# Kernel tuning notes

Measured on AMD Instinct MI355X. Metric: run time of the kernel, lower is better.

## Reference

```python
import jax, jax.numpy as jnp
import numpy as np

B, T, DM = 2, 512, 1024
H, DH = 16, 64          # n_heads, d_head = d_model // n_heads
D, R = 32, 4            # d_manifold, metric_net rank
TEMP_MIN = 0.5


def _rope_tables(t_len, d_head):
    inv_freq = 1.0 / (10000.0 ** (jnp.arange(0, d_head, 2, dtype=jnp.float32) / d_head))
    t = jnp.arange(t_len, dtype=jnp.float32)
    freqs = t[:, None] * inv_freq[None, :]          # [T, d_head//2]
    emb = jnp.concatenate([freqs, freqs], axis=-1)  # [T, d_head]
    return jnp.cos(emb), jnp.sin(emb)


def _apply_rope(x, cos, sin):
    # x: [B, H, T, d_head]
    half = x.shape[-1] // 2
    x1, x2 = x[..., :half], x[..., half:]
    c1 = cos[None, None, :, :half]
    s1 = sin[None, None, :, :half]
    return jnp.concatenate([x1 * c1 - x2 * s1, x1 * s1 + x2 * c1], axis=-1)


def setup_inputs() -> dict:
    key = jax.random.key(0)
    ks = jax.random.split(key, 9)
    s = 0.02
    return {
        "x": jax.random.normal(ks[0], (B, T, DM), dtype=jnp.float32),
        "Wq": s * jax.random.normal(ks[1], (DM, DM), dtype=jnp.float32),
        "Wk": s * jax.random.normal(ks[2], (DM, DM), dtype=jnp.float32),
        "Wv": s * jax.random.normal(ks[3], (DM, DM), dtype=jnp.float32),
        "Wo": s * jax.random.normal(ks[4], (DM, DM), dtype=jnp.float32),
        "Wqm": s * jax.random.normal(ks[5], (DH, D), dtype=jnp.float32),
        "Wkm": s * jax.random.normal(ks[6], (DH, D), dtype=jnp.float32),
        "Wmetric": s * jax.random.normal(ks[7], (D, D * R), dtype=jnp.float32),
        "temperature": jnp.asarray(1.0, dtype=jnp.float32),
    }


def reference(x, Wq, Wk, Wv, Wo, Wqm, Wkm, Wmetric, temperature):
    b, t, c = x.shape
    # projections -> [B, H, T, d_head]
    def split_heads(y):
        return y.reshape(b, t, H, DH).transpose(0, 2, 1, 3)
    q = split_heads(x @ Wq)
    k = split_heads(x @ Wk)
    v = split_heads(x @ Wv)

    cos, sin = _rope_tables(t, DH)
    q = _apply_rope(q, cos, sin)
    k = _apply_rope(k, cos, sin)

    # manifold coordinates in (0,1): [B, H, T, D]
    qm = jax.nn.sigmoid(jnp.einsum('bhtd,dm->bhtm', q, Wqm))
    km = jax.nn.sigmoid(jnp.einsum('bhtd,dm->bhtm', k, Wkm))

    # low-rank metric factor U(q): [B, H, T, D, R]
    U = jnp.einsum('bhtm,mn->bhtn', qm, Wmetric).reshape(b, H, t, D, R)

    # Euclidean part: ||q_i - k_j||^2 = |q|^2 + |k|^2 - 2 q.k  -> [B,H,T,T]
    q2 = jnp.sum(qm * qm, axis=-1)
    k2 = jnp.sum(km * km, axis=-1)
    qk = jnp.einsum('bhid,bhjd->bhij', qm, km)
    dist_euc = q2[..., :, None] + k2[..., None, :] - 2.0 * qk

    # low-rank part: ||U_i^T (q_i - k_j)||^2, factorized as U_i^T q_i - U_i^T k_j
    Uq = jnp.einsum('bhidr,bhid->bhir', U, qm)          # [B,H,T,R]
    Uk = jnp.einsum('bhidr,bhjd->bhijr', U, km)         # [B,H,T,T,R]
    dist_lr = jnp.sum((Uq[:, :, :, None, :] - Uk) ** 2, axis=-1)

    dist_sq = jnp.maximum(dist_euc + dist_lr, 0.0)

    temp = jnp.maximum(temperature, TEMP_MIN)
    attn = -dist_sq / temp

    causal = jnp.triu(jnp.ones((t, t), dtype=bool), k=1)
    attn = jnp.where(causal[None, None], -jnp.inf, attn)
    attn = jax.nn.softmax(attn, axis=-1)

    out = jnp.einsum('bhij,bhjd->bhid', attn, v)        # [B,H,T,d_head]
    out = out.transpose(0, 2, 1, 3).reshape(b, t, c)
    return out @ Wo
```

## Files before the change

### kernel.cpp

```cpp
#include <hip/hip_runtime.h>
#include <cmath>

constexpr int B_  = 2;
constexpr int T_  = 512;
constexpr int DM_ = 1024;
constexpr int H_  = 16;
constexpr int DH_ = 64;
constexpr int D_  = 32;
constexpr int R_  = 4;
constexpr int BH_ = B_ * H_;

typedef __bf16 bf16x8 __attribute__((ext_vector_type(8)));
typedef float  f32x4  __attribute__((ext_vector_type(4)));
typedef unsigned short u16x8 __attribute__((ext_vector_type(8)));

__device__ __forceinline__ unsigned short f2bf(float f) {
    unsigned u = __float_as_uint(f);
    return (unsigned short)((u + 0x7fffu + ((u >> 16) & 1u)) >> 16);
}
__device__ __forceinline__ float bf2f(unsigned short v) {
    return __uint_as_float((unsigned)v << 16);
}
__device__ __forceinline__ void gload16(const void* g, void* l) {
    __builtin_amdgcn_global_load_lds(
        (const __attribute__((address_space(1))) void*)g,
        (__attribute__((address_space(3))) void*)l, 16, 0, 0);
}

__global__ __launch_bounds__(256) void prep_kernel(
    const float* __restrict__ x,
    const float* __restrict__ Wq, const float* __restrict__ Wk,
    const float* __restrict__ Wv, const float* __restrict__ Wo,
    unsigned short* __restrict__ xb,
    unsigned short* __restrict__ wqb, unsigned short* __restrict__ wkb,
    unsigned short* __restrict__ wvb, unsigned short* __restrict__ wob)
{
    const int t = threadIdx.x;
    const int z = blockIdx.z;
    if (z == 4) {
        int base = (blockIdx.y * 16 + blockIdx.x) * 4096 + t * 16;
#pragma unroll
        for (int c = 0; c < 4; ++c) {
            float4 v = *(const float4*)&x[base + c * 4];
            ushort4 o = { f2bf(v.x), f2bf(v.y), f2bf(v.z), f2bf(v.w) };
            *(ushort4*)&xb[base + c * 4] = o;
        }
        return;
    }
    __shared__ __align__(16) unsigned short Ls[64][72];
    const float* W = (z == 0) ? Wq : (z == 1) ? Wk : (z == 2) ? Wv : Wo;
    unsigned short* O = (z == 0) ? wqb : (z == 1) ? wkb : (z == 2) ? wvb : wob;
    const int k0 = blockIdx.x * 64;
    const int n0 = blockIdx.y * 64;
#pragma unroll
    for (int it = 0; it < 4; ++it) {
        int r = it * 16 + (t >> 4);
        int c = (t & 15) * 4;
        float4 v4 = *(const float4*)&W[(size_t)(k0 + r) * DM_ + n0 + c];
        Ls[c + 0][r] = f2bf(v4.x); Ls[c + 1][r] = f2bf(v4.y);
        Ls[c + 2][r] = f2bf(v4.z); Ls[c + 3][r] = f2bf(v4.w);
    }
    __syncthreads();
#pragma unroll
    for (int it = 0; it < 2; ++it) {
        int nl = it * 32 + (t >> 3);
        int kc = (t & 7) * 8;
        *(u16x8*)&O[(size_t)(n0 + nl) * DM_ + k0 + kc] = *(const u16x8*)&Ls[nl][kc];
    }
}

__global__ __launch_bounds__(256) void gemm_qkv(
    const unsigned short* __restrict__ A,
    const unsigned short* __restrict__ Bt0,
    const unsigned short* __restrict__ Bt1,
    const unsigned short* __restrict__ Bt2,
    float* __restrict__ C0, float* __restrict__ C1,
    unsigned short* __restrict__ vT)
{
    __shared__ __align__(16) unsigned short As[2][128 * 64];
    __shared__ __align__(16) unsigned short Bs[2][128 * 64];
    const int tid  = threadIdx.x;
    const int lane = tid & 63;
    const int w    = tid >> 6;
    const int wm   = (w & 1) * 64;
    const int wn   = (w >> 1) * 64;
    const int l15  = lane & 15, quad = lane >> 4;

    const int bm = blockIdx.y * 128;
    const int n0 = blockIdx.x * 128;
    const int which = n0 >> 10;
    const int bn = n0 & 1023;
    const unsigned short* Bt = (which == 0) ? Bt0 : (which == 1) ? Bt1 : Bt2;

    const int srow = tid >> 3, kcs = tid & 7, kcg = kcs ^ (srow & 7);
    const unsigned short* Ap = A  + (size_t)(bm + srow) * DM_ + kcg * 8;
    const unsigned short* Bp = Bt + (size_t)(bn + srow) * DM_ + kcg * 8;

#pragma unroll
    for (int p = 0; p < 4; ++p) {
        gload16(Ap + (size_t)p * 32 * DM_, &As[0][tid * 8 + p * 2048]);
        gload16(Bp + (size_t)p * 32 * DM_, &Bs[0][tid * 8 + p * 2048]);
    }

    f32x4 acc[4][4] = {};
#pragma unroll
    for (int k = 0; k < 16; ++k) {
        const int cur = k & 1, nxt = cur ^ 1;
        __builtin_amdgcn_s_barrier();
        if (k + 1 < 16) {
            const int off = (k + 1) * 64;
#pragma unroll
            for (int p = 0; p < 4; ++p) {
                gload16(Ap + (size_t)p * 32 * DM_ + off, &As[nxt][tid * 8 + p * 2048]);
                gload16(Bp + (size_t)p * 32 * DM_ + off, &Bs[nxt][tid * 8 + p * 2048]);
            }
            __builtin_amdgcn_s_waitcnt(0x0F78);
        } else {
            __builtin_amdgcn_s_waitcnt(0x0F70);
        }
        __builtin_amdgcn_s_barrier();

#pragma unroll
        for (int ki = 0; ki < 2; ++ki) {
            const int kch = ki * 4 + quad;
            bf16x8 af[4], bfr[4];
#pragma unroll
            for (int i = 0; i < 4; ++i) {
                int ra = wm + i * 16 + l15;
                int rb = wn + i * 16 + l15;
                af[i]  = *(const bf16x8*)&As[cur][ra * 64 + (kch ^ (ra & 7)) * 8];
                bfr[i] = *(const bf16x8*)&Bs[cur][rb * 64 + (kch ^ (rb & 7)) * 8];
            }
#pragma unroll
            for (int mi = 0; mi < 4; ++mi)
#pragma unroll
                for (int ni = 0; ni < 4; ++ni)
                    acc[mi][ni] = __builtin_amdgcn_mfma_f32_16x16x32_bf16(
                        af[mi], bfr[ni], acc[mi][ni], 0, 0, 0);
        }
    }

#pragma unroll
    for (int mi = 0; mi < 4; ++mi)
#pragma unroll
        for (int ni = 0; ni < 4; ++ni) {
            f32x4 a = acc[mi][ni];
            int col = wn + ni * 16 + l15;
            int h = (bn + col) >> 6;
            int d = col & 63;
#pragma unroll
            for (int r = 0; r < 4; ++r) {
                int row = bm + wm + mi * 16 + quad * 4 + r;
                int bb = row >> 9, tt = row & (T_ - 1);
                if (which == 2) {
                    vT[(((size_t)bb * H_ + h) * DH_ + d) * T_ + tt] = f2bf(a[r]);
                } else {
                    float* C = (which == 0) ? C0 : C1;
                    C[(((size_t)bb * H_ + h) * T_ + tt) * DH_ + d] = a[r];
                }
            }
        }
}

__global__ __launch_bounds__(256) void gemm_out(
    const unsigned short* __restrict__ A,
    const unsigned short* __restrict__ Bt,
    float* __restrict__ C0)
{
    __shared__ __align__(16) unsigned short As[2][64 * 64];
    __shared__ __align__(16) unsigned short Bs[2][64 * 64];
    const int tid  = threadIdx.x;
    const int lane = tid & 63;
    const int w    = tid >> 6;
    const int wm   = (w & 1) * 32;
    const int wn   = (w >> 1) * 32;
    const int l15  = lane & 15, quad = lane >> 4;

    const int bm = blockIdx.y * 64;
    const int bn = blockIdx.x * 64;

    const int srow = tid >> 3, kcs = tid & 7, kcg = kcs ^ (srow & 7);
    const unsigned short* Ap0 = A  + (size_t)(bm + srow) * DM_ + kcg * 8;
    const unsigned short* Bp0 = Bt + (size_t)(bn + srow) * DM_ + kcg * 8;
    const unsigned short* Ap1 = Ap0 + 32 * DM_;
    const unsigned short* Bp1 = Bp0 + 32 * DM_;

    gload16(Ap0, &As[0][tid * 8]);
    gload16(Ap1, &As[0][tid * 8 + 2048]);
    gload16(Bp0, &Bs[0][tid * 8]);
    gload16(Bp1, &Bs[0][tid * 8 + 2048]);

    f32x4 acc[2][2] = {};
#pragma unroll
    for (int k = 0; k < 16; ++k) {
        const int cur = k & 1, nxt = cur ^ 1;
        __builtin_amdgcn_s_barrier();
        if (k + 1 < 16) {
            const int off = (k + 1) * 64;
            gload16(Ap0 + off, &As[nxt][tid * 8]);
            gload16(Ap1 + off, &As[nxt][tid * 8 + 2048]);
            gload16(Bp0 + off, &Bs[nxt][tid * 8]);
            gload16(Bp1 + off, &Bs[nxt][tid * 8 + 2048]);
            __builtin_amdgcn_s_waitcnt(0x0F74);
        } else {
            __builtin_amdgcn_s_waitcnt(0x0F70);
        }
        __builtin_amdgcn_s_barrier();

        bf16x8 af[2][2], bfr[2][2];
#pragma unroll
        for (int ki = 0; ki < 2; ++ki)
#pragma unroll
            for (int i = 0; i < 2; ++i) {
                int ra = wm + i * 16 + l15;
                int rb = wn + i * 16 + l15;
                int kch = ki * 4 + quad;
                af[ki][i]  = *(const bf16x8*)&As[cur][ra * 64 + (kch ^ (ra & 7)) * 8];
                bfr[ki][i] = *(const bf16x8*)&Bs[cur][rb * 64 + (kch ^ (rb & 7)) * 8];
            }
#pragma unroll
        for (int mi = 0; mi < 2; ++mi)
#pragma unroll
            for (int ni = 0; ni < 2; ++ni) {
                acc[mi][ni] = __builtin_amdgcn_mfma_f32_16x16x32_bf16(
                    af[0][mi], bfr[0][ni], acc[mi][ni], 0, 0, 0);
                acc[mi][ni] = __builtin_amdgcn_mfma_f32_16x16x32_bf16(
                    af[1][mi], bfr[1][ni], acc[mi][ni], 0, 0, 0);
            }
    }

#pragma unroll
    for (int mi = 0; mi < 2; ++mi)
#pragma unroll
        for (int ni = 0; ni < 2; ++ni) {
            f32x4 a = acc[mi][ni];
            int col = wn + ni * 16 + l15;
#pragma unroll
            for (int r = 0; r < 4; ++r) {
                int row = bm + wm + mi * 16 + quad * 4 + r;
                C0[(size_t)row * DM_ + bn + col] = a[r];
            }
        }
}

__global__ __launch_bounds__(256) void feat_both(
    const float* __restrict__ q_raw, const float* __restrict__ k_raw,
    const float* __restrict__ Wqm,   const float* __restrict__ Wkm,
    const float* __restrict__ Wmetric,
    unsigned short* __restrict__ a_hi, unsigned short* __restrict__ a_lo,
    unsigned short* __restrict__ km_hi, unsigned short* __restrict__ km_lo,
    float* __restrict__ q2p, float* __restrict__ k2,
    unsigned short* __restrict__ Urb)
{
    const bool QSIDE = (blockIdx.y == 0);
    const float* raw = QSIDE ? q_raw : k_raw;
    const float* Wm  = QSIDE ? Wqm   : Wkm;

    __shared__ float qrs[4][64];
    __shared__ float qms[4][32];
    const int tid  = threadIdx.x;
    const int w    = tid >> 6;
    const int lane = tid & 63;
    const int row  = blockIdx.x * 4 + w;
    const int t    = row & (T_ - 1);
    const int bh   = row >> 9;

    const int m  = lane & 31;
    const int hh = lane >> 5;

    float rv = raw[(size_t)row * 64 + lane];
    float ang = (float)t * expf((float)m * -0.28782313662425575f);
    float s, c;
    sincosf(ang, &s, &c);
    float partner = __shfl_xor(rv, 32);
    float qr = (lane < 32) ? (rv * c - partner * s) : (partner * s + rv * c);
    qrs[w][lane] = qr;

    float acc = 0.f;
#pragma unroll 8
    for (int i = 0; i < 32; ++i) {
        int d = hh * 32 + i;
        acc += qrs[w][d] * Wm[d * 32 + m];
    }
    acc += __shfl_xor(acc, 32);
    const float qm = 1.0f / (1.0f + __expf(-acc));
    if (hh == 0) qms[w][m] = qm;

    if (!QSIDE) {
        if (lane < 32) {
            unsigned short hi = f2bf(qm);
            unsigned short lo = f2bf(qm - bf2f(hi));
            size_t off = (size_t)row * 32 + lane;
            km_hi[off] = hi; km_lo[off] = lo;
        }
        float sq = (lane < 32) ? qm * qm : 0.f;
        sq += __shfl_xor(sq, 32); sq += __shfl_xor(sq, 16);
        sq += __shfl_xor(sq, 8);  sq += __shfl_xor(sq, 4);
        sq += __shfl_xor(sq, 2);  sq += __shfl_xor(sq, 1);
        if (lane == 0) k2[row] = sq;
        return;
    }

    float a0 = 0.f, a1 = 0.f;
#pragma unroll 8
    for (int mm = 0; mm < 32; ++mm) {
        float qv = qms[w][mm];
        float2 wv = *(const float2*)&Wmetric[mm * 128 + lane * 2];
        a0 += qv * wv.x;
        a1 += qv * wv.y;
    }

    {
        int n0i = lane * 2;
        int r0 = n0i & 3, d0 = n0i >> 2;
        Urb[(((size_t)bh * R_ + r0    ) * T_ + t) * D_ + d0] = f2bf(a0);
        Urb[(((size_t)bh * R_ + r0 + 1) * T_ + t) * D_ + d0] = f2bf(a1);
    }

    float dq = qms[w][lane >> 1];
    float u0 = a0 * dq, u1 = a1 * dq;
    u0 += __shfl_xor(u0, 2);  u1 += __shfl_xor(u1, 2);
    u0 += __shfl_xor(u0, 4);  u1 += __shfl_xor(u1, 4);
    u0 += __shfl_xor(u0, 8);  u1 += __shfl_xor(u1, 8);
    u0 += __shfl_xor(u0, 16); u1 += __shfl_xor(u1, 16);
    u0 += __shfl_xor(u0, 32); u1 += __shfl_xor(u1, 32);
    float v0 = __shfl_xor(u0, 1), v1 = __shfl_xor(u1, 1);
    const bool odd = (lane & 1);
    float Uq0 = odd ? v0 : u0;
    float Uq1 = odd ? v1 : u1;
    float Uq2 = odd ? u0 : v0;
    float Uq3 = odd ? u1 : v1;

    {
        int src = m * 2;
        float s0 = __shfl(a0, src);
        float s1 = __shfl(a1, src);
        float s2 = __shfl(a0, src + 1);
        float s3 = __shfl(a1, src + 1);
        if (lane < 32) {
            float b = Uq0 * s0 + Uq1 * s1 + Uq2 * s2 + Uq3 * s3;
            float a = qm + b;
            unsigned short hi = f2bf(a);
            unsigned short lo = f2bf(a - bf2f(hi));
            size_t off = (size_t)row * 32 + lane;
            a_hi[off] = hi; a_lo[off] = lo;
        }
    }

    float sq = (lane < 32) ? qm * qm : 0.f;
    sq += __shfl_xor(sq, 32); sq += __shfl_xor(sq, 16);
    sq += __shfl_xor(sq, 8);  sq += __shfl_xor(sq, 4);
    sq += __shfl_xor(sq, 2);  sq += __shfl_xor(sq, 1);
    if (lane == 0)
        q2p[row] = sq + Uq0 * Uq0 + Uq1 * Uq1 + Uq2 * Uq2 + Uq3 * Uq3;
}

constexpr int PROW = 40;
__global__ __launch_bounds__(256) void attn_mfma(
    const unsigned short* __restrict__ a_hi, const unsigned short* __restrict__ a_lo,
    const unsigned short* __restrict__ km_hi, const unsigned short* __restrict__ km_lo,
    const unsigned short* __restrict__ Urb,
    const float* __restrict__ q2p, const float* __restrict__ k2,
    const float* __restrict__ temp_p, const unsigned short* __restrict__ vT,
    unsigned short* __restrict__ ctxb)
{
    __shared__ __align__(16) unsigned short P_lds[4][32 * PROW];
    __shared__ __align__(16) float OP[4][32][64];
    __shared__ float ML[4][32];

    const int itile = blockIdx.x, bh = blockIdx.y;
    const int i0 = itile * 32;
    const int tid = threadIdx.x, w = tid >> 6, lane = tid & 63;
    const int l15 = lane & 15, quad = lane >> 4;

    const float inv_temp = 1.0f / fmaxf(temp_p[0], 0.5f);

    bf16x8 Ahi[2], Alo[2], Aur[4][2];
#pragma unroll
    for (int mi = 0; mi < 2; ++mi) {
        size_t ab = ((size_t)bh * T_ + i0 + mi * 16 + l15) * 32 + quad * 8;
        Ahi[mi] = *(const bf16x8*)&a_hi[ab];
        Alo[mi] = *(const bf16x8*)&a_lo[ab];
#pragma unroll
        for (int r = 0; r < 4; ++r)
            Aur[r][mi] = *(const bf16x8*)
                &Urb[(((size_t)bh * R_ + r) * T_ + i0 + mi * 16 + l15) * 32 + quad * 8];
    }
    float q2r[2][4];
#pragma unroll
    for (int mi = 0; mi < 2; ++mi)
#pragma unroll
        for (int rg = 0; rg < 4; ++rg)
            q2r[mi][rg] = q2p[(size_t)bh * T_ + i0 + mi * 16 + quad * 4 + rg];

    f32x4 Oacc[2][4] = {};
    float psum[2][4] = {};

    for (int jt = w; jt <= itile; jt += 4) {
        const int j0 = jt * 32;
        bf16x8 Bhi[2], Blo[2];
#pragma unroll
        for (int ni = 0; ni < 2; ++ni) {
            size_t kb = ((size_t)bh * T_ + j0 + ni * 16 + l15) * 32 + quad * 8;
            Bhi[ni] = *(const bf16x8*)&km_hi[kb];
            Blo[ni] = *(const bf16x8*)&km_lo[kb];
        }
        f32x4 acc[2][2] = {};
#pragma unroll
        for (int mi = 0; mi < 2; ++mi)
#pragma unroll
            for (int ni = 0; ni < 2; ++ni) {
                acc[mi][ni] = __builtin_amdgcn_mfma_f32_16x16x32_bf16(
                    Alo[mi], Bhi[ni], acc[mi][ni], 0, 0, 0);
                acc[mi][ni] = __builtin_amdgcn_mfma_f32_16x16x32_bf16(
                    Ahi[mi], Blo[ni], acc[mi][ni], 0, 0, 0);
                acc[mi][ni] = __builtin_amdgcn_mfma_f32_16x16x32_bf16(
                    Ahi[mi], Bhi[ni], acc[mi][ni], 0, 0, 0);
            }
        f32x4 sq[2][2] = {};
#pragma unroll
        for (int r = 0; r < 4; ++r) {
            f32x4 ar[2][2] = {};
#pragma unroll
            for (int mi = 0; mi < 2; ++mi)
#pragma unroll
                for (int ni = 0; ni < 2; ++ni)
                    ar[mi][ni] = __builtin_amdgcn_mfma_f32_16x16x32_bf16(
                        Aur[r][mi], Bhi[ni], ar[mi][ni], 0, 0, 0);
#pragma unroll
            for (int mi = 0; mi < 2; ++mi)
#pragma unroll
                for (int ni = 0; ni < 2; ++ni)
                    sq[mi][ni] += ar[mi][ni] * ar[mi][ni];
        }
        float k2c[2];
#pragma unroll
        for (int ni = 0; ni < 2; ++ni)
            k2c[ni] = k2[(size_t)bh * T_ + j0 + ni * 16 + l15];
        const bool diag = (jt == itile);
#pragma unroll
        for (int mi = 0; mi < 2; ++mi)
#pragma unroll
            for (int ni = 0; ni < 2; ++ni)
#pragma unroll
                for (int rg = 0; rg < 4; ++rg) {
                    float dist = q2r[mi][rg] + k2c[ni]
                               - 2.f * acc[mi][ni][rg] + sq[mi][ni][rg];
                    float sc = -fmaxf(dist, 0.f) * inv_temp;
                    if (diag && (ni * 16 + l15) > (mi * 16 + quad * 4 + rg))
                        sc = -1e30f;
                    float p = __expf(sc);
                    psum[mi][rg] += p;
                    P_lds[w][(mi * 16 + quad * 4 + rg) * PROW + ni * 16 + l15] = f2bf(p);
                }
        bf16x8 Pf[2], Vf[4];
#pragma unroll
        for (int mi = 0; mi < 2; ++mi)
            Pf[mi] = *(const bf16x8*)&P_lds[w][(mi * 16 + l15) * PROW + quad * 8];
#pragma unroll
        for (int n4 = 0; n4 < 4; ++n4)
            Vf[n4] = *(const bf16x8*)
                &vT[((size_t)bh * DH_ + n4 * 16 + l15) * T_ + j0 + quad * 8];
#pragma unroll
        for (int mi = 0; mi < 2; ++mi)
#pragma unroll
            for (int n4 = 0; n4 < 4; ++n4)
                Oacc[mi][n4] = __builtin_amdgcn_mfma_f32_16x16x32_bf16(
                    Pf[mi], Vf[n4], Oacc[mi][n4], 0, 0, 0);
    }

#pragma unroll
    for (int mi = 0; mi < 2; ++mi)
#pragma unroll
        for (int rg = 0; rg < 4; ++rg) {
            float v = psum[mi][rg];
            v += __shfl_xor(v, 1); v += __shfl_xor(v, 2);
            v += __shfl_xor(v, 4); v += __shfl_xor(v, 8);
            psum[mi][rg] = v;
        }
    if (l15 == 0)
#pragma unroll
        for (int mi = 0; mi < 2; ++mi)
#pragma unroll
            for (int rg = 0; rg < 4; ++rg)
                ML[w][mi * 16 + quad * 4 + rg] = psum[mi][rg];
#pragma unroll
    for (int mi = 0; mi < 2; ++mi)
#pragma unroll
        for (int n4 = 0; n4 < 4; ++n4)
#pragma unroll
            for (int rg = 0; rg < 4; ++rg)
                OP[w][mi * 16 + quad * 4 + rg][n4 * 16 + l15] = Oacc[mi][n4][rg];
    __syncthreads();

    const int ii = tid >> 3, ds = tid & 7;
    float l = ML[0][ii] + ML[1][ii] + ML[2][ii] + ML[3][ii];
    float O[8] = {};
#pragma unroll
    for (int wv = 0; wv < 4; ++wv) {
        float4 o0 = *(const float4*)&OP[wv][ii][ds * 8];
        float4 o1 = *(const float4*)&OP[wv][ii][ds * 8 + 4];
        O[0] += o0.x; O[1] += o0.y; O[2] += o0.z; O[3] += o0.w;
        O[4] += o1.x; O[5] += o1.y; O[6] += o1.z; O[7] += o1.w;
    }
    const float inv = 1.0f / l;
    const int b = bh >> 4, h = bh & 15;
    u16x8 o;
#pragma unroll
    for (int dd = 0; dd < 8; ++dd) o[dd] = f2bf(O[dd] * inv);
    *(u16x8*)&ctxb[((size_t)b * T_ + i0 + ii) * DM_ + h * 64 + ds * 8] = o;
}

extern "C" void kernel_launch(void* const* d_in, const int* in_sizes, int n_in,
                              void* d_out, int out_size, void* d_ws, size_t ws_size,
                              hipStream_t stream)
{
    const float* x       = (const float*)d_in[0];
    const float* Wq      = (const float*)d_in[1];
    const float* Wk      = (const float*)d_in[2];
    const float* Wv      = (const float*)d_in[3];
    const float* Wo      = (const float*)d_in[4];
    const float* Wqm     = (const float*)d_in[5];
    const float* Wkm     = (const float*)d_in[6];
    const float* Wmetric = (const float*)d_in[7];
    const float* temp    = (const float*)d_in[8];
    float* out = (float*)d_out;
    float* ws  = (float*)d_ws;

    float* q_raw = ws;
    float* k_raw = q_raw + (size_t)BH_ * T_ * DH_;
    float* q2p   = k_raw + (size_t)BH_ * T_ * DH_;
    float* k2    = q2p   + (size_t)BH_ * T_;
    unsigned short* xb   = (unsigned short*)(k2 + (size_t)BH_ * T_);
    unsigned short* wqb  = xb   + (size_t)DM_ * DM_;
    unsigned short* wkb  = wqb  + (size_t)DM_ * DM_;
    unsigned short* wvb  = wkb  + (size_t)DM_ * DM_;
    unsigned short* wob  = wvb  + (size_t)DM_ * DM_;
    unsigned short* a_hi = wob  + (size_t)DM_ * DM_;
    unsigned short* a_lo = a_hi + (size_t)BH_ * T_ * D_;
    unsigned short* kmhi = a_lo + (size_t)BH_ * T_ * D_;
    unsigned short* kmlo = kmhi + (size_t)BH_ * T_ * D_;
    unsigned short* Urb  = kmlo + (size_t)BH_ * T_ * D_;
    unsigned short* vT   = Urb  + (size_t)BH_ * R_ * T_ * D_;
    unsigned short* ctxb = (unsigned short*)q_raw;

    prep_kernel<<<dim3(16, 16, 5), 256, 0, stream>>>(
        x, Wq, Wk, Wv, Wo, xb, wqb, wkb, wvb, wob);
    gemm_qkv<<<dim3(24, 8), 256, 0, stream>>>(
        xb, wqb, wkb, wvb, q_raw, k_raw, vT);
    feat_both<<<dim3(BH_ * T_ / 4, 2), 256, 0, stream>>>(
        q_raw, k_raw, Wqm, Wkm, Wmetric,
        a_hi, a_lo, kmhi, kmlo, q2p, k2, Urb);
    attn_mfma<<<dim3(T_ / 32, BH_), 256, 0, stream>>>(
        a_hi, a_lo, kmhi, kmlo, Urb, q2p, k2, temp, vT, ctxb);
    gemm_out<<<dim3(16, 16), 256, 0, stream>>>(
        ctxb, wob, out);
}
```

Before: 155.3 us.

## Shrink QKV GEMM tiles to 64x64 with K=128 steps and triple-buffer output GEMM

The QKV projection GEMM moves from 128x128 tiles over a 24x8 grid to 64x64 tiles over a 48x16 grid. Each iteration now loads a K-slice of 128 split into two 64-wide halves, which halves the loop count. This is meant to raise occupancy and fill more of the MI355X's compute units than 192 blocks can, at the cost of less operand reuse per tile. The output GEMM switches from double to triple buffering, prefetching two stages ahead to hide global load latency, and uses more LDS to do so.

```diff
diff --git a/kernel.cpp b/kernel.cpp
--- a/kernel.cpp
+++ b/kernel.cpp
@@ -77,42 +77,48 @@
     float* __restrict__ C0, float* __restrict__ C1,
     unsigned short* __restrict__ vT)
 {
-    __shared__ __align__(16) unsigned short As[2][128 * 64];
-    __shared__ __align__(16) unsigned short Bs[2][128 * 64];
+    __shared__ __align__(16) unsigned short As[2][2][64 * 64];
+    __shared__ __align__(16) unsigned short Bs[2][2][64 * 64];
     const int tid  = threadIdx.x;
     const int lane = tid & 63;
     const int w    = tid >> 6;
-    const int wm   = (w & 1) * 64;
-    const int wn   = (w >> 1) * 64;
+    const int wm   = (w & 1) * 32;
+    const int wn   = (w >> 1) * 32;
     const int l15  = lane & 15, quad = lane >> 4;
 
-    const int bm = blockIdx.y * 128;
-    const int n0 = blockIdx.x * 128;
+    const int bm = blockIdx.y * 64;
+    const int n0 = blockIdx.x * 64;
     const int which = n0 >> 10;
     const int bn = n0 & 1023;
     const unsigned short* Bt = (which == 0) ? Bt0 : (which == 1) ? Bt1 : Bt2;
 
     const int srow = tid >> 3, kcs = tid & 7, kcg = kcs ^ (srow & 7);
-    const unsigned short* Ap = A  + (size_t)(bm + srow) * DM_ + kcg * 8;
-    const unsigned short* Bp = Bt + (size_t)(bn + srow) * DM_ + kcg * 8;
-
-#pragma unroll
-    for (int p = 0; p < 4; ++p) {
-        gload16(Ap + (size_t)p * 32 * DM_, &As[0][tid * 8 + p * 2048]);
-        gload16(Bp + (size_t)p * 32 * DM_, &Bs[0][tid * 8 + p * 2048]);
-    }
-
-    f32x4 acc[4][4] = {};
-#pragma unroll
-    for (int k = 0; k < 16; ++k) {
+    const unsigned short* Ap0 = A  + (size_t)(bm + srow) * DM_ + kcg * 8;
+    const unsigned short* Bp0 = Bt + (size_t)(bn + srow) * DM_ + kcg * 8;
+    const unsigned short* Ap1 = Ap0 + 32 * DM_;
+    const unsigned short* Bp1 = Bp0 + 32 * DM_;
+
+#pragma unroll
+    for (int hf = 0; hf < 2; ++hf) {
+        gload16(Ap0 + hf * 64, &As[0][hf][tid * 8]);
+        gload16(Ap1 + hf * 64, &As[0][hf][tid * 8 + 2048]);
+        gload16(Bp0 + hf * 64, &Bs[0][hf][tid * 8]);
+        gload16(Bp1 + hf * 64, &Bs[0][hf][tid * 8 + 2048]);
+    }
+
+    f32x4 acc[2][2] = {};
+#pragma unroll
+    for (int k = 0; k < 8; ++k) {
         const int cur = k & 1, nxt = cur ^ 1;
         __builtin_amdgcn_s_barrier();
-        if (k + 1 < 16) {
-            const int off = (k + 1) * 64;
-#pragma unroll
-            for (int p = 0; p < 4; ++p) {
-                gload16(Ap + (size_t)p * 32 * DM_ + off, &As[nxt][tid * 8 + p * 2048]);
-                gload16(Bp + (size_t)p * 32 * DM_ + off, &Bs[nxt][tid * 8 + p * 2048]);
+        if (k + 1 < 8) {
+            const int off = (k + 1) * 128;
+#pragma unroll
+            for (int hf = 0; hf < 2; ++hf) {
+                gload16(Ap0 + off + hf * 64, &As[nxt][hf][tid * 8]);
+                gload16(Ap1 + off + hf * 64, &As[nxt][hf][tid * 8 + 2048]);
+                gload16(Bp0 + off + hf * 64, &Bs[nxt][hf][tid * 8]);
+                gload16(Bp1 + off + hf * 64, &Bs[nxt][hf][tid * 8 + 2048]);
             }
             __builtin_amdgcn_s_waitcnt(0x0F78);
         } else {
@@ -121,33 +127,37 @@
         __builtin_amdgcn_s_barrier();
 
 #pragma unroll
-        for (int ki = 0; ki < 2; ++ki) {
-            const int kch = ki * 4 + quad;
-            bf16x8 af[4], bfr[4];
-#pragma unroll
-            for (int i = 0; i < 4; ++i) {
-                int ra = wm + i * 16 + l15;
-                int rb = wn + i * 16 + l15;
-                af[i]  = *(const bf16x8*)&As[cur][ra * 64 + (kch ^ (ra & 7)) * 8];
-                bfr[i] = *(const bf16x8*)&Bs[cur][rb * 64 + (kch ^ (rb & 7)) * 8];
-            }
-#pragma unroll
-            for (int mi = 0; mi < 4; ++mi)
-#pragma unroll
-                for (int ni = 0; ni < 4; ++ni)
+        for (int hf = 0; hf < 2; ++hf) {
+            bf16x8 af[2][2], bfr[2][2];
+#pragma unroll
+            for (int ki = 0; ki < 2; ++ki)
+#pragma unroll
+                for (int i = 0; i < 2; ++i) {
+                    int ra = wm + i * 16 + l15;
+                    int rb = wn + i * 16 + l15;
+                    int kch = ki * 4 + quad;
+                    af[ki][i]  = *(const bf16x8*)&As[cur][hf][ra * 64 + (kch ^ (ra & 7)) * 8];
+                    bfr[ki][i] = *(const bf16x8*)&Bs[cur][hf][rb * 64 + (kch ^ (rb & 7)) * 8];
+                }
+#pragma unroll
+            for (int mi = 0; mi < 2; ++mi)
+#pragma unroll
+                for (int ni = 0; ni < 2; ++ni) {
                     acc[mi][ni] = __builtin_amdgcn_mfma_f32_16x16x32_bf16(
-                        af[mi], bfr[ni], acc[mi][ni], 0, 0, 0);
-        }
-    }
-
-#pragma unroll
-    for (int mi = 0; mi < 4; ++mi)
-#pragma unroll
-        for (int ni = 0; ni < 4; ++ni) {
+                        af[0][mi], bfr[0][ni], acc[mi][ni], 0, 0, 0);
+                    acc[mi][ni] = __builtin_amdgcn_mfma_f32_16x16x32_bf16(
+                        af[1][mi], bfr[1][ni], acc[mi][ni], 0, 0, 0);
+                }
+        }
+    }
+
+#pragma unroll
+    for (int mi = 0; mi < 2; ++mi)
+#pragma unroll
+        for (int ni = 0; ni < 2; ++ni) {
             f32x4 a = acc[mi][ni];
             int col = wn + ni * 16 + l15;
-            int h = (bn + col) >> 6;
-            int d = col & 63;
+            int h = bn >> 6, d = col;
 #pragma unroll
             for (int r = 0; r < 4; ++r) {
                 int row = bm + wm + mi * 16 + quad * 4 + r;
@@ -167,8 +177,8 @@
     const unsigned short* __restrict__ Bt,
     float* __restrict__ C0)
 {
-    __shared__ __align__(16) unsigned short As[2][64 * 64];
-    __shared__ __align__(16) unsigned short Bs[2][64 * 64];
+    __shared__ __align__(16) unsigned short As[3][64 * 64];
+    __shared__ __align__(16) unsigned short Bs[3][64 * 64];
     const int tid  = threadIdx.x;
     const int lane = tid & 63;
     const int w    = tid >> 6;
@@ -189,18 +199,24 @@
     gload16(Ap1, &As[0][tid * 8 + 2048]);
     gload16(Bp0, &Bs[0][tid * 8]);
     gload16(Bp1, &Bs[0][tid * 8 + 2048]);
+    gload16(Ap0 + 64, &As[1][tid * 8]);
+    gload16(Ap1 + 64, &As[1][tid * 8 + 2048]);
+    gload16(Bp0 + 64, &Bs[1][tid * 8]);
+    gload16(Bp1 + 64, &Bs[1][tid * 8 + 2048]);
 
     f32x4 acc[2][2] = {};
 #pragma unroll
     for (int k = 0; k < 16; ++k) {
-        const int cur = k & 1, nxt = cur ^ 1;
+        const int cur = k % 3, pre = (k + 2) % 3;
         __builtin_amdgcn_s_barrier();
-        if (k + 1 < 16) {
-            const int off = (k + 1) * 64;
-            gload16(Ap0 + off, &As[nxt][tid * 8]);
-            gload16(Ap1 + off, &As[nxt][tid * 8 + 2048]);
-            gload16(Bp0 + off, &Bs[nxt][tid * 8]);
-            gload16(Bp1 + off, &Bs[nxt][tid * 8 + 2048]);
+        if (k + 2 < 16) {
+            const int off = (k + 2) * 64;
+            gload16(Ap0 + off, &As[pre][tid * 8]);
+            gload16(Ap1 + off, &As[pre][tid * 8 + 2048]);
+            gload16(Bp0 + off, &Bs[pre][tid * 8]);
+            gload16(Bp1 + off, &Bs[pre][tid * 8 + 2048]);
+            __builtin_amdgcn_s_waitcnt(0x0F78);
+        } else if (k + 1 < 16) {
             __builtin_amdgcn_s_waitcnt(0x0F74);
         } else {
             __builtin_amdgcn_s_waitcnt(0x0F70);
@@ -546,7 +562,7 @@
 
     prep_kernel<<<dim3(16, 16, 5), 256, 0, stream>>>(
         x, Wq, Wk, Wv, Wo, xb, wqb, wkb, wvb, wob);
-    gemm_qkv<<<dim3(24, 8), 256, 0, stream>>>(
+    gemm_qkv<<<dim3(48, 16), 256, 0, stream>>>(
         xb, wqb, wkb, wvb, q_raw, k_raw, vT);
     feat_both<<<dim3(BH_ * T_ / 4, 2), 256, 0, stream>>>(
         q_raw, k_raw, Wqm, Wkm, Wmetric,
```

Measured after the change: 150.3 us. 3.2% less time.

## Shrink QKV GEMM tiles to 64x64 and remap blocks across XCDs

Applied to the files above, without the earlier changes.

The fused QKV projection GEMM now uses 64x64 output tiles instead of 128x128, raising the grid from 192 to 768 workgroups so more of the GPU's compute units get work. A 1D grid with an XCD-aware index remap groups neighbouring tiles onto the same chiplet, which is meant to improve L2 reuse of the A and B panels. Each tile now fits inside one head, so the head index is computed once per block. Smaller tiles lower the ratio of MFMA work to global loads per block and add more per-block overhead.

```diff
diff --git a/kernel.cpp b/kernel.cpp
--- a/kernel.cpp
+++ b/kernel.cpp
@@ -77,77 +77,80 @@
     float* __restrict__ C0, float* __restrict__ C1,
     unsigned short* __restrict__ vT)
 {
-    __shared__ __align__(16) unsigned short As[2][128 * 64];
-    __shared__ __align__(16) unsigned short Bs[2][128 * 64];
+    __shared__ __align__(16) unsigned short As[2][64 * 64];
+    __shared__ __align__(16) unsigned short Bs[2][64 * 64];
     const int tid  = threadIdx.x;
     const int lane = tid & 63;
     const int w    = tid >> 6;
-    const int wm   = (w & 1) * 64;
-    const int wn   = (w >> 1) * 64;
+    const int wm   = (w & 1) * 32;
+    const int wn   = (w >> 1) * 32;
     const int l15  = lane & 15, quad = lane >> 4;
 
-    const int bm = blockIdx.y * 128;
-    const int n0 = blockIdx.x * 128;
+    const int wg   = (blockIdx.x & 7) * 96 + (blockIdx.x >> 3);
+    const int bm   = (wg & 15) * 64;
+    const int nidx = wg >> 4;
+    const int n0   = nidx * 64;
     const int which = n0 >> 10;
-    const int bn = n0 & 1023;
+    const int bn   = n0 & 1023;
     const unsigned short* Bt = (which == 0) ? Bt0 : (which == 1) ? Bt1 : Bt2;
 
     const int srow = tid >> 3, kcs = tid & 7, kcg = kcs ^ (srow & 7);
-    const unsigned short* Ap = A  + (size_t)(bm + srow) * DM_ + kcg * 8;
-    const unsigned short* Bp = Bt + (size_t)(bn + srow) * DM_ + kcg * 8;
-
-#pragma unroll
-    for (int p = 0; p < 4; ++p) {
-        gload16(Ap + (size_t)p * 32 * DM_, &As[0][tid * 8 + p * 2048]);
-        gload16(Bp + (size_t)p * 32 * DM_, &Bs[0][tid * 8 + p * 2048]);
-    }
-
-    f32x4 acc[4][4] = {};
+    const unsigned short* Ap0 = A  + (size_t)(bm + srow) * DM_ + kcg * 8;
+    const unsigned short* Bp0 = Bt + (size_t)(bn + srow) * DM_ + kcg * 8;
+    const unsigned short* Ap1 = Ap0 + 32 * DM_;
+    const unsigned short* Bp1 = Bp0 + 32 * DM_;
+
+    gload16(Ap0, &As[0][tid * 8]);
+    gload16(Ap1, &As[0][tid * 8 + 2048]);
+    gload16(Bp0, &Bs[0][tid * 8]);
+    gload16(Bp1, &Bs[0][tid * 8 + 2048]);
+
+    f32x4 acc[2][2] = {};
 #pragma unroll
     for (int k = 0; k < 16; ++k) {
         const int cur = k & 1, nxt = cur ^ 1;
         __builtin_amdgcn_s_barrier();
         if (k + 1 < 16) {
             const int off = (k + 1) * 64;
-#pragma unroll
-            for (int p = 0; p < 4; ++p) {
-                gload16(Ap + (size_t)p * 32 * DM_ + off, &As[nxt][tid * 8 + p * 2048]);
-                gload16(Bp + (size_t)p * 32 * DM_ + off, &Bs[nxt][tid * 8 + p * 2048]);
-            }
-            __builtin_amdgcn_s_waitcnt(0x0F78);
+            gload16(Ap0 + off, &As[nxt][tid * 8]);
+            gload16(Ap1 + off, &As[nxt][tid * 8 + 2048]);
+            gload16(Bp0 + off, &Bs[nxt][tid * 8]);
+            gload16(Bp1 + off, &Bs[nxt][tid * 8 + 2048]);
+            __builtin_amdgcn_s_waitcnt(0x0F74);
         } else {
             __builtin_amdgcn_s_waitcnt(0x0F70);
         }
         __builtin_amdgcn_s_barrier();
 
-#pragma unroll
-        for (int ki = 0; ki < 2; ++ki) {
-            const int kch = ki * 4 + quad;
-            bf16x8 af[4], bfr[4];
-#pragma unroll
-            for (int i = 0; i < 4; ++i) {
+        bf16x8 af[2][2], bfr[2][2];
+#pragma unroll
+        for (int ki = 0; ki < 2; ++ki)
+#pragma unroll
+            for (int i = 0; i < 2; ++i) {
                 int ra = wm + i * 16 + l15;
                 int rb = wn + i * 16 + l15;
-                af[i]  = *(const bf16x8*)&As[cur][ra * 64 + (kch ^ (ra & 7)) * 8];
-                bfr[i] = *(const bf16x8*)&Bs[cur][rb * 64 + (kch ^ (rb & 7)) * 8];
-            }
-#pragma unroll
-            for (int mi = 0; mi < 4; ++mi)
-#pragma unroll
-                for (int ni = 0; ni < 4; ++ni)
-                    acc[mi][ni] = __builtin_amdgcn_mfma_f32_16x16x32_bf16(
-                        af[mi], bfr[ni], acc[mi][ni], 0, 0, 0);
-        }
-    }
-
-#pragma unroll
-    for (int mi = 0; mi < 4; ++mi)
-#pragma unroll
-        for (int ni = 0; ni < 4; ++ni) {
+                int kch = ki * 4 + quad;
+                af[ki][i]  = *(const bf16x8*)&As[cur][ra * 64 + (kch ^ (ra & 7)) * 8];
+                bfr[ki][i] = *(const bf16x8*)&Bs[cur][rb * 64 + (kch ^ (rb & 7)) * 8];
+            }
+#pragma unroll
+        for (int mi = 0; mi < 2; ++mi)
+#pragma unroll
+            for (int ni = 0; ni < 2; ++ni) {
+                acc[mi][ni] = __builtin_amdgcn_mfma_f32_16x16x32_bf16(
+                    af[0][mi], bfr[0][ni], acc[mi][ni], 0, 0, 0);
+                acc[mi][ni] = __builtin_amdgcn_mfma_f32_16x16x32_bf16(
+                    af[1][mi], bfr[1][ni], acc[mi][ni], 0, 0, 0);
+            }
+    }
+
+#pragma unroll
+    for (int mi = 0; mi < 2; ++mi)
+#pragma unroll
+        for (int ni = 0; ni < 2; ++ni) {
             f32x4 a = acc[mi][ni];
             int col = wn + ni * 16 + l15;
-            int h = (bn + col) >> 6;
-            int d = col & 63;
+            int h = bn >> 6, d = col;
 #pragma unroll
             for (int r = 0; r < 4; ++r) {
                 int row = bm + wm + mi * 16 + quad * 4 + r;
@@ -546,7 +549,7 @@
 
     prep_kernel<<<dim3(16, 16, 5), 256, 0, stream>>>(
         x, Wq, Wk, Wv, Wo, xb, wqb, wkb, wvb, wob);
-    gemm_qkv<<<dim3(24, 8), 256, 0, stream>>>(
+    gemm_qkv<<<dim3(768), 256, 0, stream>>>(
         xb, wqb, wkb, wvb, q_raw, k_raw, vT);
     feat_both<<<dim3(BH_ * T_ / 4, 2), 256, 0, stream>>>(
         q_raw, k_raw, Wqm, Wkm, Wmetric,
```

Result: faster. 149.5 us (-3.7%).
